# Kernel optimization log

Hardware: AMD Instinct MI355X
Metric: run time of the kernel (lower is better)

The kernel has to match this reference:

```python
import jax, jax.numpy as jnp
import numpy as np

B, T, V, R = 512, 24, 32000, 32
# Scale keeps both the selected chain (factor ~ sqrt(R)*c per step) and the
# vocab-marginalized chain (factor ~ sqrt(V*R)*c per step) inside fp32 range.
CORE_SCALE = (R * np.sqrt(V)) ** -0.5


def setup_inputs() -> dict:
    key = jax.random.key(0)
    k1, k2, k3, k4 = jax.random.split(key, 4)
    y = jax.random.randint(k1, (B, T), 0, V)                      # (B, T) token ids
    alpha = jax.random.normal(k2, (1, R), dtype=jnp.float32)      # left boundary
    beta = jax.random.normal(k3, (1, R), dtype=jnp.float32)       # right boundary
    core = jax.random.normal(k4, (1, R, V, R), dtype=jnp.float32) * CORE_SCALE
    return {"y": y, "alpha": alpha, "beta": beta, "core": core}


def _mps_fwd(alpha, beta, core, y):
    a = alpha[0]                                   # (R,)
    b = beta[0]                                    # (R,)
    cores = jnp.transpose(core[0], (1, 0, 2))      # (V, R, R): per-token transfer matrices
    bsz, seq = y.shape

    # --- unnormalized p(y): chain of selected R x R matrices (marginalize_mask = 0) ---
    sel = jnp.moveaxis(cores[y], 1, 0)             # (T, B, R, R) gathered transfer matrices
    init = jnp.broadcast_to(a, (bsz, R))           # (B, R)

    def step(state, M):                            # state: (B, R), M: (B, R, R)
        return jnp.einsum('br,brs->bs', state, M), None

    state, _ = jax.lax.scan(step, init, sel)
    p_tilde = state @ b                            # (B,)

    # --- normalization: every position marginalized over vocab (free pos-0 leg also summed) ---
    m = cores.sum(axis=0)                          # (R, R) marginalized transfer matrix

    def zstep(v, _):                               # v: (R,)
        return v @ m, None

    vz, _ = jax.lax.scan(zstep, a, None, length=seq)
    z = (vz @ b) * bsz                             # z_one is identical per row; .sum() over batch

    return jnp.concatenate([p_tilde, z[None]])     # (B + 1,): [p_tilde..., z]


def reference(y, alpha, beta, core):
    return _mps_fwd(alpha, beta, core, y)
```

## Files before the change

kernel.cpp:

```cpp
#include <hip/hip_runtime.h>

#define RNK 32
#define VOC 32000
#define BSZ 512
#define SEQ 24

#define CHAIN_BLOCKS 128
#define REDUCE_BLOCKS 4000

__global__ __launch_bounds__(256) void fused_kernel(const float* __restrict__ core,
                                                    const int* __restrict__ y,
                                                    const float* __restrict__ alpha,
                                                    const float* __restrict__ beta,
                                                    float* __restrict__ out,
                                                    float* __restrict__ gm) {
    if (blockIdx.x < CHAIN_BLOCKS) {
        const int tid  = threadIdx.x;
        const int lane = tid & 63;
        const int s    = lane & 31;
        const int half = lane >> 5;
        const int row  = blockIdx.x * 4 + (tid >> 6);
        const size_t strideR = (size_t)VOC * RNK;
        const size_t halfOff = (size_t)half * 16 * strideR;

        int ytok = (lane < SEQ) ? y[row * SEQ + lane] : 0;

        float state = alpha[s];

        float buf[3][16];
        {
            const int tok = __shfl(ytok, 0, 64);
            const float* mb = core + (size_t)tok * RNK + s + halfOff;
            #pragma unroll
            for (int i = 0; i < 16; ++i) buf[0][i] = mb[(size_t)i * strideR];
        }
        {
            const int tok = __shfl(ytok, 1, 64);
            const float* mb = core + (size_t)tok * RNK + s + halfOff;
            #pragma unroll
            for (int i = 0; i < 16; ++i) buf[1][i] = mb[(size_t)i * strideR];
        }

        #pragma unroll
        for (int t = 0; t < SEQ; ++t) {
            if (t + 2 < SEQ) {
                const int tok = __shfl(ytok, t + 2, 64);
                const float* mb = core + (size_t)tok * RNK + s + halfOff;
                #pragma unroll
                for (int i = 0; i < 16; ++i) buf[(t + 2) % 3][i] = mb[(size_t)i * strideR];
            }
            float a0 = 0.f, a1 = 0.f, a2 = 0.f, a3 = 0.f;
            #pragma unroll
            for (int i = 0; i < 16; i += 4) {
                a0 = fmaf(__shfl(state, half * 16 + i + 0, 64), buf[t % 3][i + 0], a0);
                a1 = fmaf(__shfl(state, half * 16 + i + 1, 64), buf[t % 3][i + 1], a1);
                a2 = fmaf(__shfl(state, half * 16 + i + 2, 64), buf[t % 3][i + 2], a2);
                a3 = fmaf(__shfl(state, half * 16 + i + 3, 64), buf[t % 3][i + 3], a3);
            }
            const float acc = (a0 + a1) + (a2 + a3);
            state = acc + __shfl_xor(acc, 32, 64);
        }

        float p = state * beta[s];
        #pragma unroll
        for (int m = 16; m >= 1; m >>= 1) p += __shfl_xor(p, m, 64);
        if (lane == 0) out[row] = p;
    } else {
        const int bid   = blockIdx.x - CHAIN_BLOCKS;
        const int r     = bid & 31;
        const int chunk = bid >> 5;
        const int tid   = threadIdx.x;

        const float4* slab = (const float4*)(core + (size_t)r * VOC * RNK);
        const int base = chunk * 2048 + tid;

        float a0 = 0.f, a1 = 0.f, a2 = 0.f, a3 = 0.f;
        #pragma unroll
        for (int i = 0; i < 8; ++i) {
            float4 v = slab[base + i * 256];
            a0 += v.x; a1 += v.y; a2 += v.z; a3 += v.w;
        }

        __shared__ float ml[RNK];
        if (tid < RNK) ml[tid] = 0.f;
        __syncthreads();

        const int s0 = (tid & 7) * 4;
        atomicAdd(&ml[s0 + 0], a0);
        atomicAdd(&ml[s0 + 1], a1);
        atomicAdd(&ml[s0 + 2], a2);
        atomicAdd(&ml[s0 + 3], a3);
        __syncthreads();

        if (tid < RNK) atomicAdd(&gm[r * RNK + tid], ml[tid]);
    }
}

__global__ void zchain_kernel(const float* __restrict__ gm,
                              const float* __restrict__ alpha,
                              const float* __restrict__ beta,
                              float* __restrict__ out) {
    const int lane = threadIdx.x & 63;
    const int s    = lane & 31;
    const int half = lane >> 5;

    float col[16];
    #pragma unroll
    for (int i = 0; i < 16; ++i) col[i] = gm[(half * 16 + i) * RNK + s];

    float v = alpha[s];
    for (int t = 0; t < SEQ; ++t) {
        float a0 = 0.f, a1 = 0.f, a2 = 0.f, a3 = 0.f;
        #pragma unroll
        for (int i = 0; i < 16; i += 4) {
            a0 = fmaf(__shfl(v, half * 16 + i + 0, 64), col[i + 0], a0);
            a1 = fmaf(__shfl(v, half * 16 + i + 1, 64), col[i + 1], a1);
            a2 = fmaf(__shfl(v, half * 16 + i + 2, 64), col[i + 2], a2);
            a3 = fmaf(__shfl(v, half * 16 + i + 3, 64), col[i + 3], a3);
        }
        const float acc = (a0 + a1) + (a2 + a3);
        v = acc + __shfl_xor(acc, 32, 64);
    }
    float z = v * beta[s];
    #pragma unroll
    for (int m = 16; m >= 1; m >>= 1) z += __shfl_xor(z, m, 64);
    if (lane == 0) out[BSZ] = z * (float)BSZ;
}

extern "C" void kernel_launch(void* const* d_in, const int* in_sizes, int n_in,
                              void* d_out, int out_size, void* d_ws, size_t ws_size,
                              hipStream_t stream) {
    const int*   y     = (const int*)d_in[0];
    const float* alpha = (const float*)d_in[1];
    const float* beta  = (const float*)d_in[2];
    const float* core  = (const float*)d_in[3];
    float* out = (float*)d_out;
    float* gm  = (float*)d_ws;

    hipMemsetAsync(gm, 0, RNK * RNK * sizeof(float), stream);
    fused_kernel<<<CHAIN_BLOCKS + REDUCE_BLOCKS, 256, 0, stream>>>(core, y, alpha, beta, out, gm);
    zchain_kernel<<<1, 64, 0, stream>>>(gm, alpha, beta, out);
}
```

Baseline: 45.29 us.

## Fuse z-chain into reduction via last-block counter and deepen gather prefetch

Result: slower. 164.5 us (+263.2%).

```diff
diff --git a/kernel.cpp b/kernel.cpp
--- a/kernel.cpp
+++ b/kernel.cpp
@@ -13,7 +13,8 @@
                                                     const float* __restrict__ alpha,
                                                     const float* __restrict__ beta,
                                                     float* __restrict__ out,
-                                                    float* __restrict__ gm) {
+                                                    float* __restrict__ gm,
+                                                    unsigned* __restrict__ counter) {
     if (blockIdx.x < CHAIN_BLOCKS) {
         const int tid  = threadIdx.x;
         const int lane = tid & 63;
@@ -27,39 +28,34 @@
 
         float state = alpha[s];
 
-        float buf[3][16];
-        {
-            const int tok = __shfl(ytok, 0, 64);
-            const float* mb = core + (size_t)tok * RNK + s + halfOff;
-            #pragma unroll
-            for (int i = 0; i < 16; ++i) buf[0][i] = mb[(size_t)i * strideR];
+        float buf[5][16];
+
+#define LOADM(SLOT, T)                                                         \
+        {                                                                      \
+            const int tok = __shfl(ytok, (T), 64);                             \
+            const float* mb = core + (size_t)tok * RNK + s + halfOff;          \
+            _Pragma("unroll")                                                  \
+            for (int i = 0; i < 16; ++i) buf[SLOT][i] = mb[(size_t)i * strideR]; \
         }
-        {
-            const int tok = __shfl(ytok, 1, 64);
-            const float* mb = core + (size_t)tok * RNK + s + halfOff;
-            #pragma unroll
-            for (int i = 0; i < 16; ++i) buf[1][i] = mb[(size_t)i * strideR];
-        }
+
+        LOADM(0, 0) LOADM(1, 1) LOADM(2, 2) LOADM(3, 3)
 
         #pragma unroll
         for (int t = 0; t < SEQ; ++t) {
-            if (t + 2 < SEQ) {
-                const int tok = __shfl(ytok, t + 2, 64);
-                const float* mb = core + (size_t)tok * RNK + s + halfOff;
-                #pragma unroll
-                for (int i = 0; i < 16; ++i) buf[(t + 2) % 3][i] = mb[(size_t)i * strideR];
-            }
+            if (t + 4 < SEQ) LOADM((t + 4) % 5, t + 4)
+
             float a0 = 0.f, a1 = 0.f, a2 = 0.f, a3 = 0.f;
             #pragma unroll
             for (int i = 0; i < 16; i += 4) {
-                a0 = fmaf(__shfl(state, half * 16 + i + 0, 64), buf[t % 3][i + 0], a0);
-                a1 = fmaf(__shfl(state, half * 16 + i + 1, 64), buf[t % 3][i + 1], a1);
-                a2 = fmaf(__shfl(state, half * 16 + i + 2, 64), buf[t % 3][i + 2], a2);
-                a3 = fmaf(__shfl(state, half * 16 + i + 3, 64), buf[t % 3][i + 3], a3);
+                a0 = fmaf(__shfl(state, half * 16 + i + 0, 64), buf[t % 5][i + 0], a0);
+                a1 = fmaf(__shfl(state, half * 16 + i + 1, 64), buf[t % 5][i + 1], a1);
+                a2 = fmaf(__shfl(state, half * 16 + i + 2, 64), buf[t % 5][i + 2], a2);
+                a3 = fmaf(__shfl(state, half * 16 + i + 3, 64), buf[t % 5][i + 3], a3);
             }
             const float acc = (a0 + a1) + (a2 + a3);
             state = acc + __shfl_xor(acc, 32, 64);
         }
+#undef LOADM
 
         float p = state * beta[s];
         #pragma unroll
@@ -82,6 +78,7 @@
         }
 
         __shared__ float ml[RNK];
+        __shared__ int isLast;
         if (tid < RNK) ml[tid] = 0.f;
         __syncthreads();
 
@@ -93,38 +90,47 @@
         __syncthreads();
 
         if (tid < RNK) atomicAdd(&gm[r * RNK + tid], ml[tid]);
+
+        __syncthreads();
+        if (tid == 0) {
+            __threadfence();
+            unsigned old = atomicAdd(counter, 1u);
+            isLast = (old == REDUCE_BLOCKS - 1);
+        }
+        __syncthreads();
+
+        if (isLast && tid < 64) {
+            __threadfence();
+            const int lane = tid;
+            const int s    = lane & 31;
+            const int half = lane >> 5;
+
+            float col[16];
+            #pragma unroll
+            for (int i = 0; i < 16; ++i)
+                col[i] = __hip_atomic_load(&gm[(half * 16 + i) * RNK + s],
+                                           __ATOMIC_RELAXED, __HIP_MEMORY_SCOPE_AGENT);
+
+            float v = alpha[s];
+            #pragma unroll
+            for (int t = 0; t < SEQ; ++t) {
+                float b0 = 0.f, b1 = 0.f, b2 = 0.f, b3 = 0.f;
+                #pragma unroll
+                for (int i = 0; i < 16; i += 4) {
+                    b0 = fmaf(__shfl(v, half * 16 + i + 0, 64), col[i + 0], b0);
+                    b1 = fmaf(__shfl(v, half * 16 + i + 1, 64), col[i + 1], b1);
+                    b2 = fmaf(__shfl(v, half * 16 + i + 2, 64), col[i + 2], b2);
+                    b3 = fmaf(__shfl(v, half * 16 + i + 3, 64), col[i + 3], b3);
+                }
+                const float acc = (b0 + b1) + (b2 + b3);
+                v = acc + __shfl_xor(acc, 32, 64);
+            }
+            float z = v * beta[s];
+            #pragma unroll
+            for (int m = 16; m >= 1; m >>= 1) z += __shfl_xor(z, m, 64);
+            if (lane == 0) out[BSZ] = z * (float)BSZ;
+        }
     }
-}
-
-__global__ void zchain_kernel(const float* __restrict__ gm,
-                              const float* __restrict__ alpha,
-                              const float* __restrict__ beta,
-                              float* __restrict__ out) {
-    const int lane = threadIdx.x & 63;
-    const int s    = lane & 31;
-    const int half = lane >> 5;
-
-    float col[16];
-    #pragma unroll
-    for (int i = 0; i < 16; ++i) col[i] = gm[(half * 16 + i) * RNK + s];
-
-    float v = alpha[s];
-    for (int t = 0; t < SEQ; ++t) {
-        float a0 = 0.f, a1 = 0.f, a2 = 0.f, a3 = 0.f;
-        #pragma unroll
-        for (int i = 0; i < 16; i += 4) {
-            a0 = fmaf(__shfl(v, half * 16 + i + 0, 64), col[i + 0], a0);
-            a1 = fmaf(__shfl(v, half * 16 + i + 1, 64), col[i + 1], a1);
-            a2 = fmaf(__shfl(v, half * 16 + i + 2, 64), col[i + 2], a2);
-            a3 = fmaf(__shfl(v, half * 16 + i + 3, 64), col[i + 3], a3);
-        }
-        const float acc = (a0 + a1) + (a2 + a3);
-        v = acc + __shfl_xor(acc, 32, 64);
-    }
-    float z = v * beta[s];
-    #pragma unroll
-    for (int m = 16; m >= 1; m >>= 1) z += __shfl_xor(z, m, 64);
-    if (lane == 0) out[BSZ] = z * (float)BSZ;
 }
 
 extern "C" void kernel_launch(void* const* d_in, const int* in_sizes, int n_in,
@@ -136,8 +142,9 @@
     const float* core  = (const float*)d_in[3];
     float* out = (float*)d_out;
     float* gm  = (float*)d_ws;
+    unsigned* counter = (unsigned*)(gm + RNK * RNK);
 
-    hipMemsetAsync(gm, 0, RNK * RNK * sizeof(float), stream);
-    fused_kernel<<<CHAIN_BLOCKS + REDUCE_BLOCKS, 256, 0, stream>>>(core, y, alpha, beta, out, gm);
-    zchain_kernel<<<1, 64, 0, stream>>>(gm, alpha, beta, out);
+    hipMemsetAsync(d_ws, 0, RNK * RNK * sizeof(float) + sizeof(unsigned), stream);
+    fused_kernel<<<CHAIN_BLOCKS + REDUCE_BLOCKS, 256, 0, stream>>>(
+        core, y, alpha, beta, out, gm, counter);
 }
```

## Stream chain transfer matrices into LDS via direct global-to-LDS loads

Applied to the files above, without the earlier changes.

Measured after the change: 48.40 us. 6.9% more time.

```diff
diff --git a/kernel.cpp b/kernel.cpp
--- a/kernel.cpp
+++ b/kernel.cpp
@@ -8,60 +8,78 @@
 #define CHAIN_BLOCKS 128
 #define REDUCE_BLOCKS 4000
 
+typedef const __attribute__((address_space(1))) void* as1_cvp;
+typedef __attribute__((address_space(3))) void* as3_vp;
+
+__device__ __forceinline__ void issue_matrix_load(const float* __restrict__ src_tok,
+                                                  float* lds_base, int lane) {
+    const int r  = lane >> 3;
+    const int c0 = (lane & 7) * 4;
+    #pragma unroll
+    for (int j = 0; j < 4; ++j) {
+        const float* src = src_tok + (size_t)(j * 8 + r) * ((size_t)VOC * RNK) + c0;
+        __builtin_amdgcn_global_load_lds((as1_cvp)src, (as3_vp)(lds_base + j * 256), 16, 0, 0);
+    }
+}
+
 __global__ __launch_bounds__(256) void fused_kernel(const float* __restrict__ core,
                                                     const int* __restrict__ y,
                                                     const float* __restrict__ alpha,
                                                     const float* __restrict__ beta,
                                                     float* __restrict__ out,
                                                     float* __restrict__ gm) {
+    __shared__ float shmem[4 * 3 * 1024 + RNK];
+
     if (blockIdx.x < CHAIN_BLOCKS) {
         const int tid  = threadIdx.x;
         const int lane = tid & 63;
+        const int w    = tid >> 6;
         const int s    = lane & 31;
         const int half = lane >> 5;
-        const int row  = blockIdx.x * 4 + (tid >> 6);
-        const size_t strideR = (size_t)VOC * RNK;
-        const size_t halfOff = (size_t)half * 16 * strideR;
+        const int row  = blockIdx.x * 4 + w;
 
-        int ytok = (lane < SEQ) ? y[row * SEQ + lane] : 0;
+        float* mybuf = shmem + w * 3072;
 
+        int   ytok  = (lane < SEQ) ? y[row * SEQ + lane] : 0;
         float state = alpha[s];
+        float betav = beta[s];
 
-        float buf[3][16];
+        asm volatile("s_waitcnt vmcnt(0)" ::: "memory");
+
         {
             const int tok = __shfl(ytok, 0, 64);
-            const float* mb = core + (size_t)tok * RNK + s + halfOff;
-            #pragma unroll
-            for (int i = 0; i < 16; ++i) buf[0][i] = mb[(size_t)i * strideR];
+            issue_matrix_load(core + (size_t)tok * RNK, mybuf + 0 * 1024, lane);
         }
         {
             const int tok = __shfl(ytok, 1, 64);
-            const float* mb = core + (size_t)tok * RNK + s + halfOff;
-            #pragma unroll
-            for (int i = 0; i < 16; ++i) buf[1][i] = mb[(size_t)i * strideR];
+            issue_matrix_load(core + (size_t)tok * RNK, mybuf + 1 * 1024, lane);
         }
 
         #pragma unroll
         for (int t = 0; t < SEQ; ++t) {
+            if (t < SEQ - 1) asm volatile("s_waitcnt vmcnt(4)" ::: "memory");
+            else             asm volatile("s_waitcnt vmcnt(0)" ::: "memory");
+            __builtin_amdgcn_sched_barrier(0);
+
             if (t + 2 < SEQ) {
                 const int tok = __shfl(ytok, t + 2, 64);
-                const float* mb = core + (size_t)tok * RNK + s + halfOff;
-                #pragma unroll
-                for (int i = 0; i < 16; ++i) buf[(t + 2) % 3][i] = mb[(size_t)i * strideR];
+                issue_matrix_load(core + (size_t)tok * RNK, mybuf + ((t + 2) % 3) * 1024, lane);
             }
+
+            const float* M = mybuf + (t % 3) * 1024;
             float a0 = 0.f, a1 = 0.f, a2 = 0.f, a3 = 0.f;
             #pragma unroll
             for (int i = 0; i < 16; i += 4) {
-                a0 = fmaf(__shfl(state, half * 16 + i + 0, 64), buf[t % 3][i + 0], a0);
-                a1 = fmaf(__shfl(state, half * 16 + i + 1, 64), buf[t % 3][i + 1], a1);
-                a2 = fmaf(__shfl(state, half * 16 + i + 2, 64), buf[t % 3][i + 2], a2);
-                a3 = fmaf(__shfl(state, half * 16 + i + 3, 64), buf[t % 3][i + 3], a3);
+                a0 = fmaf(__shfl(state, half * 16 + i + 0, 64), M[(half * 16 + i + 0) * 32 + s], a0);
+                a1 = fmaf(__shfl(state, half * 16 + i + 1, 64), M[(half * 16 + i + 1) * 32 + s], a1);
+                a2 = fmaf(__shfl(state, half * 16 + i + 2, 64), M[(half * 16 + i + 2) * 32 + s], a2);
+                a3 = fmaf(__shfl(state, half * 16 + i + 3, 64), M[(half * 16 + i + 3) * 32 + s], a3);
             }
             const float acc = (a0 + a1) + (a2 + a3);
             state = acc + __shfl_xor(acc, 32, 64);
         }
 
-        float p = state * beta[s];
+        float p = state * betav;
         #pragma unroll
         for (int m = 16; m >= 1; m >>= 1) p += __shfl_xor(p, m, 64);
         if (lane == 0) out[row] = p;
@@ -81,7 +99,7 @@
             a0 += v.x; a1 += v.y; a2 += v.z; a3 += v.w;
         }
 
-        __shared__ float ml[RNK];
+        float* ml = shmem;
         if (tid < RNK) ml[tid] = 0.f;
         __syncthreads();
 
@@ -109,6 +127,7 @@
     for (int i = 0; i < 16; ++i) col[i] = gm[(half * 16 + i) * RNK + s];
 
     float v = alpha[s];
+    #pragma unroll
     for (int t = 0; t < SEQ; ++t) {
         float a0 = 0.f, a1 = 0.f, a2 = 0.f, a3 = 0.f;
         #pragma unroll
```
